# Optimization experiments

Hardware: AMD Instinct MI355X
Metric: run time of the kernel (lower is better)

The kernel has to match this reference:

```python
import jax, jax.numpy as jnp
import numpy as np

D_MODEL = 1024
NUM_HEADS = 16
D_HEAD = D_MODEL // NUM_HEADS
MAX_SEQ_LEN = 2048
THETA = 10000.0
BATCH = 2
SEQ = 2048


def _rope_tables():
    # inv_freq over even dims; emb interleaves each freq twice: [f0,f0,f1,f1,...]
    inv_freq = 1.0 / (THETA ** (jnp.arange(0, D_HEAD, 2, dtype=jnp.float32) / D_HEAD))
    t = jnp.arange(MAX_SEQ_LEN, dtype=jnp.float32)
    freqs = jnp.einsum('i,j->ij', t, inv_freq)  # [S, d_head/2]
    emb = jnp.stack((freqs, freqs), axis=-1).reshape(MAX_SEQ_LEN, D_HEAD)
    return jnp.cos(emb), jnp.sin(emb)


def _rotate_half(x):
    # pairwise interleaved rotation: (x0,x1,x2,x3,...) -> (-x1,x0,-x3,x2,...)
    xr = x.reshape(x.shape[:-1] + (D_HEAD // 2, 2))
    x1, x2 = xr[..., 0], xr[..., 1]
    return jnp.stack((-x2, x1), axis=-1).reshape(x.shape)


def setup_inputs() -> dict:
    key = jax.random.key(0)
    ks = jax.random.split(key, 5)
    std = np.sqrt(2.0 / (D_MODEL + D_MODEL)).astype(np.float32)
    return {
        'in_features': jax.random.normal(ks[0], (BATCH, SEQ, D_MODEL), dtype=jnp.float32),
        'token_positions': jnp.arange(SEQ, dtype=jnp.int64) if jax.config.jax_enable_x64 else jnp.arange(SEQ, dtype=jnp.int32),
        'wq': jax.random.normal(ks[1], (D_MODEL, D_MODEL), dtype=jnp.float32) * std,
        'wk': jax.random.normal(ks[2], (D_MODEL, D_MODEL), dtype=jnp.float32) * std,
        'wv': jax.random.normal(ks[3], (D_MODEL, D_MODEL), dtype=jnp.float32) * std,
        'wo': jax.random.normal(ks[4], (D_MODEL, D_MODEL), dtype=jnp.float32) * std,
    }


def reference(in_features, token_positions, wq, wk, wv, wo):
    b, s, _ = in_features.shape
    cos_tab, sin_tab = _rope_tables()
    cos = cos_tab[token_positions]  # [s, d_head]
    sin = sin_tab[token_positions]

    def split_heads(t):  # [b, s, d_model] -> [b, h, s, d_head]
        return t.reshape(b, s, NUM_HEADS, D_HEAD).transpose(0, 2, 1, 3)

    q = split_heads(jnp.einsum('bsd,ed->bse', in_features, wq))
    k = split_heads(jnp.einsum('bsd,ed->bse', in_features, wk))
    v = split_heads(jnp.einsum('bsd,ed->bse', in_features, wv))

    q = q * cos + _rotate_half(q) * sin
    k = k * cos + _rotate_half(k) * sin

    scale = 1.0 / np.sqrt(D_HEAD).astype(np.float32)
    scores = jnp.einsum('bhqd,bhkd->bhqk', q, k) * scale  # [b,h,s,s]
    causal = jnp.tril(jnp.ones((s, s), dtype=bool))
    scores = jnp.where(causal, scores, -jnp.inf)
    weights = jax.nn.softmax(scores, axis=-1)
    out = jnp.einsum('bhqk,bhkd->bhqd', weights, v)
    out = out.transpose(0, 2, 1, 3).reshape(b, s, D_MODEL)
    return jnp.einsum('bsd,ed->bse', out, wo)
```

## Files before the change

### kernel.cpp

```cpp
#include <hip/hip_runtime.h>


typedef __attribute__((ext_vector_type(8))) short bf16x8;
typedef __attribute__((ext_vector_type(4))) float f32x4;

__device__ __forceinline__ short f2bf(float f) {
  unsigned u = __float_as_uint(f);
  unsigned r = (u + 0x7fffu + ((u >> 16) & 1u)) >> 16;
  return (short)(r & 0xFFFFu);
}

__device__ __forceinline__ unsigned pk2(float a, float b) {
  return __builtin_amdgcn_perm(__float_as_uint(b) + 0x8000u,
                               __float_as_uint(a) + 0x8000u, 0x07060302u);
}

__device__ __forceinline__ void async16(const void* g, void* l) {
  __builtin_amdgcn_global_load_lds(
      (const __attribute__((address_space(1))) void*)g,
      (__attribute__((address_space(3))) void*)l, 16, 0, 0);
}

__device__ __forceinline__ void cstore(short* C, size_t i, float v) { C[i] = f2bf(v); }
__device__ __forceinline__ void cstore(float* C, size_t i, float v) { C[i] = v; }

__global__ void cast_all(const float4* __restrict__ X,
                         const float4* __restrict__ w0, const float4* __restrict__ w1,
                         const float4* __restrict__ w2, const float4* __restrict__ w3,
                         short* __restrict__ Xb, short* __restrict__ Wb) {
  int t = blockIdx.x * 256 + threadIdx.x;
  const float4* s;
  short4* d;
  if (t < (1 << 20)) {
    s = X + t; d = (short4*)Xb + t;
  } else {
    int u = t - (1 << 20);
    int which = u >> 18;
    s = ((which == 0) ? w0 : (which == 1) ? w1 : (which == 2) ? w2 : w3) + (u & 0x3FFFF);
    d = (short4*)Wb + u;
  }
  float4 v = *s;
  *d = make_short4(f2bf(v.x), f2bf(v.y), f2bf(v.z), f2bf(v.w));
}

enum EpiMode { EPI_ROW, EPI_KFRAG, EPI_VFRAG };

template <typename OUT, int MR, int NR, bool ROPE, EpiMode EM>
__device__ __forceinline__ void gemm_core(short* __restrict__ As, short* __restrict__ Bs,
                                          const short* __restrict__ A, const short* __restrict__ B,
                                          OUT* __restrict__ C, int bm, int bn, int ldc,
                                          const int* __restrict__ pos) {
  constexpr int BM = 32 * MR, BN = 32 * NR;
  const int tid  = threadIdx.x;
  const int lane = tid & 63, wave = tid >> 6;
  const int col  = lane & 15, quad = lane >> 4;
  const int wm = (wave & 1) * (16 * MR), wn = (wave >> 1) * (16 * NR);

  f32x4 acc[MR][NR];
#pragma unroll
  for (int i = 0; i < MR; i++)
#pragma unroll
    for (int j = 0; j < NR; j++) acc[i][j] = (f32x4){0.f, 0.f, 0.f, 0.f};

  auto stage = [&](int k0, int bu) {
#pragma unroll
    for (int c = tid; c < BM * 4; c += 256) {
      int r = c >> 2, cc = (c & 3) << 3;
      async16(A + (size_t)(bm + r) * 1024 + k0 + cc, As + bu * BM * 32 + c * 8);
    }
#pragma unroll
    for (int c = tid; c < BN * 4; c += 256) {
      int r = c >> 2, cc = (c & 3) << 3;
      async16(B + (size_t)(bn + r) * 1024 + k0 + cc, Bs + bu * BN * 32 + c * 8);
    }
  };

  stage(0, 0);
  for (int it = 0; it < 32; ++it) {
    __syncthreads();
    if (it < 31) stage((it + 1) * 32, (it + 1) & 1);
    const short* as = As + (it & 1) * BM * 32;
    const short* bs = Bs + (it & 1) * BN * 32;

    bf16x8 af[MR], bfr[NR];
#pragma unroll
    for (int i = 0; i < MR; i++)
      af[i] = *(const bf16x8*)(as + (wm + i * 16 + col) * 32 + quad * 8);
#pragma unroll
    for (int i = 0; i < NR; i++)
      bfr[i] = *(const bf16x8*)(bs + (wn + i * 16 + col) * 32 + quad * 8);
#pragma unroll
    for (int mi = 0; mi < MR; mi++)
#pragma unroll
      for (int ni = 0; ni < NR; ni++)
        acc[mi][ni] = __builtin_amdgcn_mfma_f32_16x16x32_bf16(af[mi], bfr[ni], acc[mi][ni], 0, 0, 0);
  }

  if (ROPE) {
    float invf_rev[NR];
#pragma unroll
    for (int ni = 0; ni < NR; ni++) {
      int pr = ((bn + wn + ni * 16 + col) & 63) >> 1;
      invf_rev[ni] = exp2f(-0.4152410118609203f * (float)pr) * 0.15915494309189535f;
    }
    const float sgn = (col & 1) ? 1.f : -1.f;
#pragma unroll
    for (int mi = 0; mi < MR; mi++) {
#pragma unroll
      for (int r = 0; r < 4; r++) {
        int row = bm + wm + mi * 16 + quad * 4 + r;
        float fp = (float)pos[row & 2047];
#pragma unroll
        for (int ni = 0; ni < NR; ni++) {
          float rev = fp * invf_rev[ni];
          rev -= floorf(rev);
          float sn = __builtin_amdgcn_sinf(rev);
          float cs = __builtin_amdgcn_cosf(rev);
          float x  = acc[mi][ni][r];
          float px = __shfl_xor(x, 1);
          acc[mi][ni][r] = fmaf(x, cs, sgn * px * sn);
        }
      }
    }
  }

  if (EM == EPI_ROW) {
#pragma unroll
    for (int mi = 0; mi < MR; mi++) {
#pragma unroll
      for (int r = 0; r < 4; r++) {
        size_t row = (size_t)(bm + wm + mi * 16 + quad * 4 + r);
#pragma unroll
        for (int ni = 0; ni < NR; ni++) {
          int cg = bn + wn + ni * 16 + col;
          cstore(C, row * ldc + cg, acc[mi][ni][r]);
        }
      }
    }
  } else if (EM == EPI_KFRAG) {
#pragma unroll
    for (int mi = 0; mi < MR; mi++) {
#pragma unroll
      for (int r = 0; r < 4; r++) {
        int m = bm + wm + mi * 16 + quad * 4 + r;
        int bq = m >> 11, key = m & 2047;
        int kt = key >> 6, nb = (key >> 4) & 3, cl = key & 15;
#pragma unroll
        for (int ni = 0; ni < NR; ni++) {
          int e = bn + wn + ni * 16 + col;
          int h = e >> 6, d = e & 63;
          size_t seg = ((((size_t)(bq * 16 + h) * 32 + kt) * 4 + nb) * 2 + (d >> 5));
          cstore((short*)C, seg * 512 + (((d >> 3) & 3) * 16 + cl) * 8 + (d & 7), acc[mi][ni][r]);
        }
      }
    }
  } else {
#pragma unroll
    for (int mi = 0; mi < MR; mi++) {
#pragma unroll
      for (int r = 0; r < 4; r++) {
        int e = bm + wm + mi * 16 + quad * 4 + r;
        int h = e >> 6, d = e & 63;
        int nb = d >> 4, cl = d & 15;
#pragma unroll
        for (int ni = 0; ni < NR; ni++) {
          int m = bn + wn + ni * 16 + col;
          int bq = m >> 11, key = m & 2047;
          int kt = key >> 6, k64 = key & 63;
          size_t seg = ((((size_t)(bq * 16 + h) * 32 + kt) * 4 + nb) * 2 + (k64 >> 5));
          cstore((short*)C, seg * 512 + (((k64 >> 3) & 3) * 16 + cl) * 8 + (k64 & 7), acc[mi][ni][r]);
        }
      }
    }
  }
}

__global__ __launch_bounds__(256) void qkv_gemm(const short* __restrict__ Xb,
                                                const short* __restrict__ Wq,
                                                const short* __restrict__ Wk,
                                                const short* __restrict__ Wv,
                                                short* __restrict__ Qo,
                                                short* __restrict__ Kf,
                                                short* __restrict__ Vf,
                                                const int* __restrict__ pos) {
  __shared__ __align__(16) short sm[2 * 128 * 32 + 2 * 128 * 32];
  short* As = sm;
  short* Bs = sm + 2 * 128 * 32;
  const int z = blockIdx.z;
  if (z == 0)      gemm_core<short, 4, 4, true,  EPI_ROW  >(As, Bs, Xb, Wq, Qo, blockIdx.x * 128, blockIdx.y * 128, 1024, pos);
  else if (z == 1) gemm_core<short, 4, 4, true,  EPI_KFRAG>(As, Bs, Xb, Wk, Kf, blockIdx.x * 128, blockIdx.y * 128, 0, pos);
  else             gemm_core<short, 4, 4, false, EPI_VFRAG>(As, Bs, Wv, Xb, Vf, blockIdx.y * 128, blockIdx.x * 128, 0, pos);
}

__global__ __launch_bounds__(256) void out_gemm(const short* __restrict__ Ctx,
                                                const short* __restrict__ Wo,
                                                float* __restrict__ C) {
  __shared__ __align__(16) short sm[2 * 64 * 32 + 2 * 128 * 32];
  gemm_core<float, 2, 4, false, EPI_ROW>(sm, sm + 2 * 64 * 32, Ctx, Wo, C,
                                         blockIdx.x * 64, blockIdx.y * 128, 1024, nullptr);
}

__global__ __launch_bounds__(256, 4) void flash_attn(const short* __restrict__ Q,
                                                     const short* __restrict__ Kf,
                                                     const short* __restrict__ Vf,
                                                     short* __restrict__ ctx) {
  const int y = blockIdx.y;
  const int qt = (y & 1) ? (31 - (y >> 1)) : (y >> 1);
  const int bh = blockIdx.x;
  const int b = bh >> 4, h = bh & 15;
  __shared__ __align__(16) short Ps[4][16 * 72];
  const int tid = threadIdx.x, lane = tid & 63, wave = tid >> 6;
  const int col = lane & 15, quad = lane >> 4;

  const short* Kfb = Kf + (size_t)bh * 131072 + lane * 8;
  const short* Vfb = Vf + (size_t)bh * 131072 + lane * 8;

  auto ldk = [&](int kt, bf16x8 (&kf)[4][2]) {
    const int base = kt * 4096;
#pragma unroll
    for (int nb = 0; nb < 4; nb++) {
      kf[nb][0] = *(const bf16x8*)(Kfb + base + (nb * 2 + 0) * 512);
      kf[nb][1] = *(const bf16x8*)(Kfb + base + (nb * 2 + 1) * 512);
    }
  };
  auto ldv = [&](int kt, bf16x8 (&vf)[4][2]) {
    const int base = kt * 4096;
#pragma unroll
    for (int nb = 0; nb < 4; nb++) {
      vf[nb][0] = *(const bf16x8*)(Vfb + base + (nb * 2 + 0) * 512);
      vf[nb][1] = *(const bf16x8*)(Vfb + base + (nb * 2 + 1) * 512);
    }
  };

  bf16x8 kf[4][2], vf[4][2];
  ldk(0, kf);

  const size_t qrow = (size_t)(b * 2048 + qt * 64 + wave * 16 + col);
  bf16x8 qf0 = *(const bf16x8*)(Q + qrow * 1024 + h * 64 + quad * 8);
  bf16x8 qf1 = *(const bf16x8*)(Q + qrow * 1024 + h * 64 + 32 + quad * 8);

  float l_i = 0.f;
  f32x4 o_acc[4];
#pragma unroll
  for (int i = 0; i < 4; i++) o_acc[i] = (f32x4){0.f, 0.f, 0.f, 0.f};

  const float C1 = 0.18033688011112042f;
  const float C2 = 17.31234049066756f;
  const int qg = qt * 64 + wave * 16 + col;

  short* myPs = &Ps[wave][0];
  const int pswr = col * 72;
  const int psrd = col * 72 + quad * 8;

  for (int kt = 0; kt <= qt; ++kt) {
    ldv(kt, vf);
    f32x4 s_acc[4];
#pragma unroll
    for (int nb = 0; nb < 4; nb++) {
      f32x4 z = (f32x4){0.f, 0.f, 0.f, 0.f};
      z = __builtin_amdgcn_mfma_f32_16x16x32_bf16(kf[nb][0], qf0, z, 0, 0, 0);
      z = __builtin_amdgcn_mfma_f32_16x16x32_bf16(kf[nb][1], qf1, z, 0, 0, 0);
      s_acc[nb] = z;
    }
    if (kt < qt) ldk(kt + 1, kf);
    const bool diag = (kt == qt);
#pragma unroll
    for (int nb = 0; nb < 4; nb++) {
      float p[4];
#pragma unroll
      for (int r = 0; r < 4; r++) {
        p[r] = exp2f(s_acc[nb][r] * C1 - C2);
        if (diag && (kt * 64 + nb * 16 + quad * 4 + r) > qg) p[r] = 0.f;
        l_i += p[r];
      }
      *(uint2*)(myPs + pswr + nb * 16 + quad * 4) = make_uint2(pk2(p[0], p[1]), pk2(p[2], p[3]));
    }
    bf16x8 af0 = *(const bf16x8*)(myPs + psrd);
    bf16x8 af1 = *(const bf16x8*)(myPs + psrd + 32);
#pragma unroll
    for (int nb = 0; nb < 4; nb++) {
      o_acc[nb] = __builtin_amdgcn_mfma_f32_16x16x32_bf16(af0, vf[nb][0], o_acc[nb], 0, 0, 0);
      o_acc[nb] = __builtin_amdgcn_mfma_f32_16x16x32_bf16(af1, vf[nb][1], o_acc[nb], 0, 0, 0);
    }
  }

  l_i += __shfl_xor(l_i, 16);
  l_i += __shfl_xor(l_i, 32);
  float invl = 1.0f / l_i;

#pragma unroll
  for (int r = 0; r < 4; r++) {
    float inv = __shfl(invl, quad * 4 + r);
    size_t row = (size_t)(b * 2048 + qt * 64 + wave * 16 + quad * 4 + r);
#pragma unroll
    for (int nb = 0; nb < 4; nb++)
      ctx[row * 1024 + h * 64 + nb * 16 + col] = f2bf(o_acc[nb][r] * inv);
  }
}

extern "C" void kernel_launch(void* const* d_in, const int* in_sizes, int n_in,
                              void* d_out, int out_size, void* d_ws, size_t ws_size,
                              hipStream_t stream) {
  const float* X  = (const float*)d_in[0];
  const int* pos  = (const int*)d_in[1];
  const float* wq = (const float*)d_in[2];
  const float* wk = (const float*)d_in[3];
  const float* wv = (const float*)d_in[4];
  const float* wo = (const float*)d_in[5];
  float* out = (float*)d_out;

  short* Xb  = (short*)d_ws;
  short* Wqb = Xb + (1 << 22);
  short* Wkb = Wqb + (1 << 20);
  short* Wvb = Wkb + (1 << 20);
  short* Wob = Wvb + (1 << 20);
  short* Qb  = Wob + (1 << 20);
  short* Kfb = Qb + (1 << 22);
  short* Vfb = Kfb + (1 << 22);
  short* Ctx = Vfb + (1 << 22);

  cast_all<<<8192, 256, 0, stream>>>((const float4*)X, (const float4*)wq, (const float4*)wk,
                                     (const float4*)wv, (const float4*)wo, Xb, Wqb);
  qkv_gemm<<<dim3(32, 8, 3), 256, 0, stream>>>(Xb, Wqb, Wkb, Wvb, Qb, Kfb, Vfb, pos);
  flash_attn<<<dim3(32, 32), 256, 0, stream>>>(Qb, Kfb, Vfb, Ctx);
  out_gemm<<<dim3(64, 8), 256, 0, stream>>>(Ctx, Wob, out);
}
```

Measured before the change: 196.7 us.

## Pair causal query tiles per block and swizzle P LDS layout

Each attention block now processes two query tiles, p and 31-p, so every block does the same amount of causal work. The grid is halved and launch bounds drop to 2 blocks per SM. The P scratch buffer in LDS is XOR-swizzled by column to cut bank conflicts on the packed writes and the fragment reads. The cost is fewer blocks (512), which may lower occupancy and latency hiding, and the two tiles in a block run one after the other.

```diff
diff --git a/kernel.cpp b/kernel.cpp
--- a/kernel.cpp
+++ b/kernel.cpp
@@ -200,12 +200,11 @@
                                          blockIdx.x * 64, blockIdx.y * 128, 1024, nullptr);
 }
 
-__global__ __launch_bounds__(256, 4) void flash_attn(const short* __restrict__ Q,
+__global__ __launch_bounds__(256, 2) void flash_attn(const short* __restrict__ Q,
                                                      const short* __restrict__ Kf,
                                                      const short* __restrict__ Vf,
                                                      short* __restrict__ ctx) {
-  const int y = blockIdx.y;
-  const int qt = (y & 1) ? (31 - (y >> 1)) : (y >> 1);
+  const int p = blockIdx.y;
   const int bh = blockIdx.x;
   const int b = bh >> 4, h = bh & 15;
   __shared__ __align__(16) short Ps[4][16 * 72];
@@ -215,6 +214,18 @@
   const short* Kfb = Kf + (size_t)bh * 131072 + lane * 8;
   const short* Vfb = Vf + (size_t)bh * 131072 + lane * 8;
 
+  const float C1 = 0.18033688011112042f;
+  const float C2 = 17.31234049066756f;
+
+  short* myPs = &Ps[wave][0];
+  const int cx = col & 3;
+  const int pswr0 = col * 72 + ((0 ^ cx) << 4) + quad * 4;
+  const int pswr1 = col * 72 + ((1 ^ cx) << 4) + quad * 4;
+  const int pswr2 = col * 72 + ((2 ^ cx) << 4) + quad * 4;
+  const int pswr3 = col * 72 + ((3 ^ cx) << 4) + quad * 4;
+  const int psrd0 = col * 72 + (((quad >> 1) ^ cx) << 4) + (quad & 1) * 8;
+  const int psrd1 = col * 72 + ((((quad >> 1) + 2) ^ cx) << 4) + (quad & 1) * 8;
+
   auto ldk = [&](int kt, bf16x8 (&kf)[4][2]) {
     const int base = kt * 4096;
 #pragma unroll
@@ -232,70 +243,69 @@
     }
   };
 
-  bf16x8 kf[4][2], vf[4][2];
-  ldk(0, kf);
-
-  const size_t qrow = (size_t)(b * 2048 + qt * 64 + wave * 16 + col);
-  bf16x8 qf0 = *(const bf16x8*)(Q + qrow * 1024 + h * 64 + quad * 8);
-  bf16x8 qf1 = *(const bf16x8*)(Q + qrow * 1024 + h * 64 + 32 + quad * 8);
-
-  float l_i = 0.f;
-  f32x4 o_acc[4];
-#pragma unroll
-  for (int i = 0; i < 4; i++) o_acc[i] = (f32x4){0.f, 0.f, 0.f, 0.f};
-
-  const float C1 = 0.18033688011112042f;
-  const float C2 = 17.31234049066756f;
-  const int qg = qt * 64 + wave * 16 + col;
-
-  short* myPs = &Ps[wave][0];
-  const int pswr = col * 72;
-  const int psrd = col * 72 + quad * 8;
-
-  for (int kt = 0; kt <= qt; ++kt) {
-    ldv(kt, vf);
-    f32x4 s_acc[4];
-#pragma unroll
-    for (int nb = 0; nb < 4; nb++) {
-      f32x4 z = (f32x4){0.f, 0.f, 0.f, 0.f};
-      z = __builtin_amdgcn_mfma_f32_16x16x32_bf16(kf[nb][0], qf0, z, 0, 0, 0);
-      z = __builtin_amdgcn_mfma_f32_16x16x32_bf16(kf[nb][1], qf1, z, 0, 0, 0);
-      s_acc[nb] = z;
-    }
-    if (kt < qt) ldk(kt + 1, kf);
-    const bool diag = (kt == qt);
-#pragma unroll
-    for (int nb = 0; nb < 4; nb++) {
-      float p[4];
-#pragma unroll
-      for (int r = 0; r < 4; r++) {
-        p[r] = exp2f(s_acc[nb][r] * C1 - C2);
-        if (diag && (kt * 64 + nb * 16 + quad * 4 + r) > qg) p[r] = 0.f;
-        l_i += p[r];
-      }
-      *(uint2*)(myPs + pswr + nb * 16 + quad * 4) = make_uint2(pk2(p[0], p[1]), pk2(p[2], p[3]));
-    }
-    bf16x8 af0 = *(const bf16x8*)(myPs + psrd);
-    bf16x8 af1 = *(const bf16x8*)(myPs + psrd + 32);
-#pragma unroll
-    for (int nb = 0; nb < 4; nb++) {
-      o_acc[nb] = __builtin_amdgcn_mfma_f32_16x16x32_bf16(af0, vf[nb][0], o_acc[nb], 0, 0, 0);
-      o_acc[nb] = __builtin_amdgcn_mfma_f32_16x16x32_bf16(af1, vf[nb][1], o_acc[nb], 0, 0, 0);
-    }
-  }
-
-  l_i += __shfl_xor(l_i, 16);
-  l_i += __shfl_xor(l_i, 32);
-  float invl = 1.0f / l_i;
-
-#pragma unroll
-  for (int r = 0; r < 4; r++) {
-    float inv = __shfl(invl, quad * 4 + r);
-    size_t row = (size_t)(b * 2048 + qt * 64 + wave * 16 + quad * 4 + r);
-#pragma unroll
-    for (int nb = 0; nb < 4; nb++)
-      ctx[row * 1024 + h * 64 + nb * 16 + col] = f2bf(o_acc[nb][r] * inv);
-  }
+  auto process = [&](int qt) {
+    const size_t qrow = (size_t)(b * 2048 + qt * 64 + wave * 16 + col);
+    bf16x8 qf0 = *(const bf16x8*)(Q + qrow * 1024 + h * 64 + quad * 8);
+    bf16x8 qf1 = *(const bf16x8*)(Q + qrow * 1024 + h * 64 + 32 + quad * 8);
+
+    float l_i = 0.f;
+    f32x4 o_acc[4];
+#pragma unroll
+    for (int i = 0; i < 4; i++) o_acc[i] = (f32x4){0.f, 0.f, 0.f, 0.f};
+
+    const int qg = qt * 64 + wave * 16 + col;
+    bf16x8 kf[4][2], vf[4][2];
+    ldk(0, kf);
+
+    for (int kt = 0; kt <= qt; ++kt) {
+      ldv(kt, vf);
+      f32x4 s_acc[4];
+#pragma unroll
+      for (int nb = 0; nb < 4; nb++) {
+        f32x4 z = (f32x4){0.f, 0.f, 0.f, 0.f};
+        z = __builtin_amdgcn_mfma_f32_16x16x32_bf16(kf[nb][0], qf0, z, 0, 0, 0);
+        z = __builtin_amdgcn_mfma_f32_16x16x32_bf16(kf[nb][1], qf1, z, 0, 0, 0);
+        s_acc[nb] = z;
+      }
+      if (kt < qt) ldk(kt + 1, kf);
+      const bool diag = (kt == qt);
+#pragma unroll
+      for (int nb = 0; nb < 4; nb++) {
+        float pv[4];
+#pragma unroll
+        for (int r = 0; r < 4; r++) {
+          pv[r] = exp2f(s_acc[nb][r] * C1 - C2);
+          if (diag && (kt * 64 + nb * 16 + quad * 4 + r) > qg) pv[r] = 0.f;
+          l_i += pv[r];
+        }
+        int wr = (nb == 0) ? pswr0 : (nb == 1) ? pswr1 : (nb == 2) ? pswr2 : pswr3;
+        *(uint2*)(myPs + wr) = make_uint2(pk2(pv[0], pv[1]), pk2(pv[2], pv[3]));
+      }
+      bf16x8 af0 = *(const bf16x8*)(myPs + psrd0);
+      bf16x8 af1 = *(const bf16x8*)(myPs + psrd1);
+#pragma unroll
+      for (int nb = 0; nb < 4; nb++) {
+        o_acc[nb] = __builtin_amdgcn_mfma_f32_16x16x32_bf16(af0, vf[nb][0], o_acc[nb], 0, 0, 0);
+        o_acc[nb] = __builtin_amdgcn_mfma_f32_16x16x32_bf16(af1, vf[nb][1], o_acc[nb], 0, 0, 0);
+      }
+    }
+
+    l_i += __shfl_xor(l_i, 16);
+    l_i += __shfl_xor(l_i, 32);
+    float invl = 1.0f / l_i;
+
+#pragma unroll
+    for (int r = 0; r < 4; r++) {
+      float inv = __shfl(invl, quad * 4 + r);
+      size_t row = (size_t)(b * 2048 + qt * 64 + wave * 16 + quad * 4 + r);
+#pragma unroll
+      for (int nb = 0; nb < 4; nb++)
+        ctx[row * 1024 + h * 64 + nb * 16 + col] = f2bf(o_acc[nb][r] * inv);
+    }
+  };
+
+  process(p);
+  process(31 - p);
 }
 
 extern "C" void kernel_launch(void* const* d_in, const int* in_sizes, int n_in,
@@ -322,6 +332,6 @@
   cast_all<<<8192, 256, 0, stream>>>((const float4*)X, (const float4*)wq, (const float4*)wk,
                                      (const float4*)wv, (const float4*)wo, Xb, Wqb);
   qkv_gemm<<<dim3(32, 8, 3), 256, 0, stream>>>(Xb, Wqb, Wkb, Wvb, Qb, Kfb, Vfb, pos);
-  flash_attn<<<dim3(32, 32), 256, 0, stream>>>(Qb, Kfb, Vfb, Ctx);
+  flash_attn<<<dim3(32, 16), 256, 0, stream>>>(Qb, Kfb, Vfb, Ctx);
   out_gemm<<<dim3(64, 8), 256, 0, stream>>>(Ctx, Wob, out);
 }
```

Result: faster. 182.8 us (-7.1%).
